# Optimization experiments

Measured on AMD Instinct MI355X. Metric: run time of the kernel, lower is better.

Reference implementation:

```python
import jax, jax.numpy as jnp
import numpy as np

B, T, X_DIM, H_DIM, C_NUM = 64, 1380, 96, 192, 345
SCALE = 1.0 / (X_DIM ** 0.5 * H_DIM ** 0.5)


def setup_inputs() -> dict:
    key = jax.random.key(0)
    k1, k2, k3, k4 = jax.random.split(key, 4)
    X = jax.random.normal(k1, (B, T, X_DIM), dtype=jnp.float32)
    H = jax.random.normal(k2, (B, T, H_DIM), dtype=jnp.float32)
    W1 = jax.random.normal(k3, (X_DIM, H_DIM), dtype=jnp.float32)
    W2 = jax.random.normal(k4, (C_NUM, T), dtype=jnp.float32)
    return {"X": X, "H": H, "W1": W1, "W2": W2}


def reference(X, H, W1, W2):
    # X: [B,T,x_dim] -> project to h_dim
    Xp = jnp.einsum('btx,xh->bth', X, W1)                 # [B,T,h]
    # batch_dot(X, H, axes=[2,2]) / sqrt(x_dim*h_dim)
    A = jnp.einsum('bth,buh->btu', Xp, H) * SCALE         # [B,T,T]
    # K.dot(W2, A) -> [c,B,T], then permute (1,0,2) -> [B,c,T]
    A = jnp.einsum('ct,btu->bcu', W2, A)                  # [B,c,T]
    A = jax.nn.softmax(A, axis=-1)
    # batch_dot(A, H, axes=[2,1])
    C = jnp.einsum('bcu,buh->bch', A, H)                  # [B,c,h]
    return C
```

## Files before the change

### kernel.cpp

```cpp
#include <hip/hip_runtime.h>
#include <math.h>

namespace {
constexpr int B_  = 64;
constexpr int T_  = 1380;
constexpr int XD_ = 96;
constexpr int HD_ = 192;
constexpr int CN_ = 345;
constexpr int CP_ = 384;
constexpr int TP_ = 1392;
constexpr int TP2_ = 1408;
constexpr int TH_ = 690;
constexpr float SCALE_ = 0.00736569563735987f;
}

typedef __attribute__((ext_vector_type(8))) short bf16x8;
typedef __attribute__((ext_vector_type(4))) float f32x4;
typedef unsigned short u16;
typedef unsigned int   u32;

__device__ __forceinline__ u16 f2bf(float f) {
    union { float f; u32 u; } c; c.f = f;
    u32 r = (c.u + 0x7fffu + ((c.u >> 16) & 1u)) >> 16;
    return (u16)r;
}
__device__ __forceinline__ float bf2f(u16 s) {
    union { u32 u; float f; } c; c.u = ((u32)s) << 16;
    return c.f;
}

__device__ __forceinline__ float red16_max(float v) {
    int ti;
    ti = __builtin_amdgcn_update_dpp(0, __builtin_bit_cast(int, v), 0x128, 0xf, 0xf, true);
    v = fmaxf(v, __builtin_bit_cast(float, ti));
    ti = __builtin_amdgcn_update_dpp(0, __builtin_bit_cast(int, v), 0x124, 0xf, 0xf, true);
    v = fmaxf(v, __builtin_bit_cast(float, ti));
    ti = __builtin_amdgcn_update_dpp(0, __builtin_bit_cast(int, v), 0x122, 0xf, 0xf, true);
    v = fmaxf(v, __builtin_bit_cast(float, ti));
    ti = __builtin_amdgcn_update_dpp(0, __builtin_bit_cast(int, v), 0x121, 0xf, 0xf, true);
    v = fmaxf(v, __builtin_bit_cast(float, ti));
    return v;
}
__device__ __forceinline__ float red16_sum(float v) {
    int ti;
    ti = __builtin_amdgcn_update_dpp(0, __builtin_bit_cast(int, v), 0x128, 0xf, 0xf, true);
    v += __builtin_bit_cast(float, ti);
    ti = __builtin_amdgcn_update_dpp(0, __builtin_bit_cast(int, v), 0x124, 0xf, 0xf, true);
    v += __builtin_bit_cast(float, ti);
    ti = __builtin_amdgcn_update_dpp(0, __builtin_bit_cast(int, v), 0x122, 0xf, 0xf, true);
    v += __builtin_bit_cast(float, ti);
    ti = __builtin_amdgcn_update_dpp(0, __builtin_bit_cast(int, v), 0x121, 0xf, 0xf, true);
    v += __builtin_bit_cast(float, ti);
    return v;
}

__global__ __launch_bounds__(256) void k0_h(const float* __restrict__ Hg,
                                            u16* __restrict__ Hh,
                                            u16* __restrict__ Hl,
                                            u16* __restrict__ Hth) {
    __shared__ u16 til[64][68];
    const int tid = threadIdx.x;
    const int u0 = blockIdx.x * 64, h0 = blockIdx.y * 64, b = blockIdx.z;
#pragma unroll
    for (int i = 0; i < 8; i++) {
        int lin = i * 256 + tid;
        int r = lin >> 5;
        int cp = lin & 31;
        int u = u0 + r, h = h0 + cp * 2;
        float2 v = make_float2(0.f, 0.f);
        if (u < T_) v = *(const float2*)(Hg + ((size_t)b * T_ + u) * HD_ + h);
        u16 hx = f2bf(v.x), hy = f2bf(v.y);
        u16 lx = f2bf(v.x - bf2f(hx)), ly = f2bf(v.y - bf2f(hy));
        if (u < T_) {
            *(u32*)(Hh + ((size_t)b * T_ + u) * HD_ + h) = (u32)hx | ((u32)hy << 16);
            *(u32*)(Hl + ((size_t)b * T_ + u) * HD_ + h) = (u32)lx | ((u32)ly << 16);
        }
        til[cp * 2][r]     = hx;
        til[cp * 2 + 1][r] = hy;
    }
    __syncthreads();
#pragma unroll
    for (int i = 0; i < 4; i++) {
        int lin = i * 256 + tid;
        int hh = lin >> 4, cc = lin & 15;
        int u = u0 + cc * 4;
        if (u + 4 <= T_) {
            ushort4 v;
            v.x = til[hh][cc * 4 + 0];
            v.y = til[hh][cc * 4 + 1];
            v.z = til[hh][cc * 4 + 2];
            v.w = til[hh][cc * 4 + 3];
            *(ushort4*)(Hth + ((size_t)b * HD_ + h0 + hh) * TP_ + u) = v;
        }
    }
}

__global__ __launch_bounds__(256) void k0_x(const float* __restrict__ Xg,
                                            u16* __restrict__ Xth,
                                            u16* __restrict__ Xtl) {
    __shared__ __align__(16) u16 tih[96][72];
    __shared__ __align__(16) u16 til[96][72];
    const int tid = threadIdx.x;
    const int t0 = blockIdx.x * 64, b = blockIdx.y;
#pragma unroll
    for (int i = 0; i < 24; i++) {
        int lin = i * 256 + tid;
        int r = lin / 96, x = lin % 96;
        float v = (t0 + r < T_) ? Xg[((size_t)b * T_ + t0 + r) * XD_ + x] : 0.f;
        u16 hi = f2bf(v);
        tih[x][r] = hi;
        til[x][r] = f2bf(v - bf2f(hi));
    }
    __syncthreads();
#pragma unroll
    for (int i = 0; i < 6; i++) {
        int id = i * 256 + tid;
        int buf = (id >= 768);
        int cid = buf ? id - 768 : id;
        int x = cid >> 3, col = cid & 7;
        uint4 v = *(const uint4*)&(buf ? til : tih)[x][col * 8];
        u16* dst = (buf ? Xtl : Xth) + ((size_t)b * XD_ + x) * TP2_ + t0 + col * 8;
        *(uint4*)dst = v;
    }
}

__global__ __launch_bounds__(256) void k0_w2(const float* __restrict__ W2g,
                                             u16* __restrict__ W2h,
                                             u16* __restrict__ W2l) {
    const int n = CP_ * (TP2_ / 2);
    for (int i = blockIdx.x * 256 + threadIdx.x; i < n; i += gridDim.x * 256) {
        int c = i / (TP2_ / 2), tc = i % (TP2_ / 2);
        int t = tc * 2;
        float v0 = 0.f, v1 = 0.f;
        if (c < CN_) {
            if (t < T_)     v0 = W2g[(size_t)c * T_ + t];
            if (t + 1 < T_) v1 = W2g[(size_t)c * T_ + t + 1];
        }
        u16 h0 = f2bf(v0), h1 = f2bf(v1);
        u16 l0 = f2bf(v0 - bf2f(h0)), l1 = f2bf(v1 - bf2f(h1));
        ((u32*)W2h)[i] = (u32)h0 | ((u32)h1 << 16);
        ((u32*)W2l)[i] = (u32)l0 | ((u32)l1 << 16);
    }
}

__global__ __launch_bounds__(256) void k0_w1(const float* __restrict__ W1g,
                                             u16* __restrict__ W1th,
                                             u16* __restrict__ W1tl) {
    int i = blockIdx.x * 256 + threadIdx.x;
    if (i < HD_ * XD_) {
        int h = i / XD_, x = i % XD_;
        float v = W1g[(size_t)x * HD_ + h];
        u16 hi = f2bf(v);
        W1th[i] = hi;
        W1tl[i] = f2bf(v - bf2f(hi));
    }
}

__global__ __launch_bounds__(256, 1) void k12_mfma(const u16* __restrict__ W2h,
                                                   const u16* __restrict__ W2l,
                                                   const u16* __restrict__ Xth,
                                                   const u16* __restrict__ Xtl,
                                                   const u16* __restrict__ W1th,
                                                   const u16* __restrict__ W1tl,
                                                   u32* __restrict__ Ysi) {
    __shared__ __align__(16) u16 smem[49152];
    float* sZ = (float*)smem;

    const int tid  = threadIdx.x;
    const int lane = tid & 63;
    const int w    = tid >> 6;
    const int tx   = lane & 15;
    const int quad = lane >> 4;
    const int wr   = w >> 1;
    const int wc2  = w & 1;
    const int L    = blockIdx.x;
    const int xcd  = L & 7;
    const int slot = L >> 3;
    const int b    = xcd * 8 + (slot >> 2);
    const int c0   = (slot & 3) * 96;

    const u16* gsrc;
    size_t rowstart;
    if (w == 0)      { gsrc = W2h; rowstart = (size_t)c0; }
    else if (w == 1) { gsrc = W2l; rowstart = (size_t)c0; }
    else if (w == 2) { gsrc = Xth; rowstart = (size_t)b * XD_; }
    else             { gsrc = Xtl; rowstart = (size_t)b * XD_; }
    const int jg = (lane & 7) ^ ((lane >> 3) & 7);

#define STAGE(bufsel, kk)                                                         \
    {                                                                             \
        u16* lb = smem + (bufsel) * 24576 + w * 6144;                             \
        _Pragma("unroll")                                                         \
        for (int i_ = 0; i_ < 12; i_++) {                                         \
            int row_ = i_ * 8 + (lane >> 3);                                      \
            const u16* gp_ = gsrc + (rowstart + row_) * TP2_ + (kk) + jg * 8;     \
            __builtin_amdgcn_global_load_lds(                                     \
                (const __attribute__((address_space(1))) u32*)(const void*)gp_,   \
                (__attribute__((address_space(3))) u32*)(void*)(lb + i_ * 512),   \
                16, 0, 0);                                                        \
        }                                                                         \
    }

    f32x4 accZ[3][3];
#pragma unroll
    for (int i = 0; i < 3; i++)
#pragma unroll
        for (int j = 0; j < 3; j++) accZ[i][j] = (f32x4){0.f, 0.f, 0.f, 0.f};

    STAGE(0, 0);
    for (int s = 0; s < 22; s++) {
        __builtin_amdgcn_sched_barrier(0);
        if (s < 21) {
            STAGE((s + 1) & 1, (s + 1) * 64);
            asm volatile("s_waitcnt vmcnt(12)" ::: "memory");
        } else {
            asm volatile("s_waitcnt vmcnt(0)" ::: "memory");
        }
        __builtin_amdgcn_s_barrier();
        __builtin_amdgcn_sched_barrier(0);
        const u16* bufp = smem + (s & 1) * 24576;
#pragma unroll
        for (int ks2 = 0; ks2 < 2; ks2++) {
            const int G = ks2 * 4 + quad;
            bf16x8 ah[3], al[3], bh3[3], bl3[3];
#pragma unroll
            for (int am = 0; am < 3; am++) {
                int row = wr * 48 + am * 16 + tx;
                int off = row * 64 + (G ^ (row & 7)) * 8;
                ah[am] = *(const bf16x8*)(bufp + off);
                al[am] = *(const bf16x8*)(bufp + 6144 + off);
            }
#pragma unroll
            for (int bn = 0; bn < 3; bn++) {
                int row = wc2 * 48 + bn * 16 + tx;
                int off = row * 64 + (G ^ (row & 7)) * 8;
                bh3[bn] = *(const bf16x8*)(bufp + 12288 + off);
                bl3[bn] = *(const bf16x8*)(bufp + 18432 + off);
            }
#pragma unroll
            for (int am = 0; am < 3; am++)
#pragma unroll
                for (int bn = 0; bn < 3; bn++) {
                    accZ[am][bn] = __builtin_amdgcn_mfma_f32_16x16x32_bf16(ah[am], bh3[bn], accZ[am][bn], 0, 0, 0);
                    accZ[am][bn] = __builtin_amdgcn_mfma_f32_16x16x32_bf16(ah[am], bl3[bn], accZ[am][bn], 0, 0, 0);
                    accZ[am][bn] = __builtin_amdgcn_mfma_f32_16x16x32_bf16(al[am], bh3[bn], accZ[am][bn], 0, 0, 0);
                }
        }
        asm volatile("s_waitcnt lgkmcnt(0)" ::: "memory");
        __builtin_amdgcn_sched_barrier(0);
        __builtin_amdgcn_s_barrier();
    }
#undef STAGE

    __builtin_amdgcn_sched_barrier(0);
#pragma unroll
    for (int am = 0; am < 3; am++)
#pragma unroll
        for (int bn = 0; bn < 3; bn++)
#pragma unroll
            for (int r = 0; r < 4; r++)
                sZ[(wr * 48 + am * 16 + quad * 4 + r) * 100 + wc2 * 48 + bn * 16 + tx] = accZ[am][bn][r];
    __syncthreads();

    bf16x8 A2h[3][3], A2l[3][3];
#pragma unroll
    for (int am = 0; am < 3; am++)
#pragma unroll
        for (int ks = 0; ks < 3; ks++) {
            const float* zrow = sZ + (wr * 48 + am * 16 + tx) * 100 + ks * 32 + quad * 8;
            bf16x8 vh, vl;
#pragma unroll
            for (int j = 0; j < 8; j++) {
                float v = zrow[j];
                u16 hi = f2bf(v);
                vh[j] = (short)hi;
                vl[j] = (short)f2bf(v - bf2f(hi));
            }
            A2h[am][ks] = vh; A2l[am][ks] = vl;
        }

    f32x4 accY[3][6];
#pragma unroll
    for (int i = 0; i < 3; i++)
#pragma unroll
        for (int j = 0; j < 6; j++) accY[i][j] = (f32x4){0.f, 0.f, 0.f, 0.f};
#pragma unroll
    for (int hn = 0; hn < 6; hn++) {
        const int hrow = wc2 * 96 + hn * 16 + tx;
#pragma unroll
        for (int ks = 0; ks < 3; ks++) {
            bf16x8 bh = *(const bf16x8*)(W1th + (size_t)hrow * XD_ + ks * 32 + quad * 8);
            bf16x8 bl = *(const bf16x8*)(W1tl + (size_t)hrow * XD_ + ks * 32 + quad * 8);
#pragma unroll
            for (int am = 0; am < 3; am++) {
                accY[am][hn] = __builtin_amdgcn_mfma_f32_16x16x32_bf16(A2h[am][ks], bh, accY[am][hn], 0, 0, 0);
                accY[am][hn] = __builtin_amdgcn_mfma_f32_16x16x32_bf16(A2h[am][ks], bl, accY[am][hn], 0, 0, 0);
                accY[am][hn] = __builtin_amdgcn_mfma_f32_16x16x32_bf16(A2l[am][ks], bh, accY[am][hn], 0, 0, 0);
            }
        }
    }

#pragma unroll
    for (int am = 0; am < 3; am++)
#pragma unroll
        for (int r = 0; r < 4; r++) {
            int c = c0 + wr * 48 + am * 16 + quad * 4 + r;
            if (c < CN_) {
                size_t base = ((size_t)b * CN_ + c) * HD_;
#pragma unroll
                for (int hn = 0; hn < 6; hn++) {
                    float y = SCALE_ * accY[am][hn][r];
                    u16 hi = f2bf(y);
                    u16 lo = f2bf(y - bf2f(hi));
                    Ysi[base + wc2 * 96 + hn * 16 + tx] = (u32)hi | ((u32)lo << 16);
                }
            }
        }
}

__global__ __launch_bounds__(768, 3) void k3_mfma(const u32* __restrict__ Ysi,
                                                  const u16* __restrict__ Hh,
                                                  const u16* __restrict__ Hl,
                                                  const u16* __restrict__ Hth,
                                                  float* __restrict__ Op,
                                                  float* __restrict__ Ml,
                                                  float* __restrict__ Ll) {
    __shared__ __align__(16) u16 smem[44544];

    const int tid  = threadIdx.x;
    const int lane = tid & 63;
    const int w    = tid >> 6;
    const int tx   = lane & 15;
    const int quad = lane >> 4;
    const int L    = blockIdx.x;
    const int xcd  = L & 7;
    const int slot = L >> 3;
    const int gp   = xcd * 16 + (slot >> 1);
    const int ct   = slot & 1;
    const int b    = gp >> 1;
    const int sp   = gp & 1;
    const int c0   = ct * 192;
    const int us   = sp * TH_, ue = us + TH_;

    bf16x8 Ah[6], Al[6];
    const int ar = c0 + w * 16 + tx;
    if (ar < CN_) {
        const u32* yi = Ysi + ((size_t)b * CN_ + ar) * HD_;
#pragma unroll
        for (int ks = 0; ks < 6; ks++) {
            u32 vv[8];
            *(uint4*)&vv[0] = *(const uint4*)(yi + ks * 32 + quad * 8);
            *(uint4*)&vv[4] = *(const uint4*)(yi + ks * 32 + quad * 8 + 4);
            bf16x8 hh, ll;
#pragma unroll
            for (int j = 0; j < 8; j++) {
                hh[j] = (short)(vv[j] & 0xffffu);
                ll[j] = (short)(vv[j] >> 16);
            }
            Ah[ks] = hh; Al[ks] = ll;
        }
    } else {
#pragma unroll
        for (int ks = 0; ks < 6; ks++) { Ah[ks] = (bf16x8)0; Al[ks] = (bf16x8)0; }
    }

    float m_s[4], l_s[4];
    f32x4 accO[12];
#pragma unroll
    for (int r = 0; r < 4; r++) { m_s[r] = -1e30f; l_s[r] = 0.f; }
#pragma unroll
    for (int j = 0; j < 12; j++) accO[j] = (f32x4){0.f, 0.f, 0.f, 0.f};

    const char* srcp[3];
    u32 off0[3];
    const u32 incw = (u32)__builtin_amdgcn_readfirstlane((w < 8) ? (32 * HD_ * 2) : 64);
#pragma unroll
    for (int j = 0; j < 3; j++) {
        int k = w * 3 + j;
        u32 o;
        if (k < 24) {
            int arr = (k < 12) ? 0 : 1;
            int ii  = k - arr * 12;
            int cid = ii * 64 + lane;
            int u   = cid / 24, c1 = cid % 24;
            int c   = (c1 & ~7) | ((c1 & 7) ^ ((u >> 1) & 7));
            const u16* basep = (arr == 0 ? Hh : Hl) + (size_t)b * T_ * HD_;
            srcp[j] = (const char*)basep + ((size_t)(us + u) * HD_ + c * 8) * 2;
            o = (u32)(arr * 24576 + ii * 1024);
        } else {
            int ii  = k - 24;
            int cid = ii * 64 + lane;
            int h   = cid >> 2, c2 = cid & 3;
            int c   = c2 ^ ((h >> 2) & 3);
            const u16* basep = Hth + (size_t)b * HD_ * TP_;
            srcp[j] = (const char*)basep + ((size_t)h * TP_ + us + c * 8) * 2;
            o = (u32)(49152 + ii * 1024);
        }
        off0[j] = (u32)__builtin_amdgcn_readfirstlane((int)o);
    }

#define STAGE3(bufsel)                                                            \
    {                                                                             \
        _Pragma("unroll")                                                         \
        for (int j_ = 0; j_ < 3; j_++) {                                          \
            __builtin_amdgcn_global_load_lds(                                     \
                (const __attribute__((address_space(1))) u32*)(const void*)srcp[j_], \
                (__attribute__((address_space(3))) u32*)(void*)((char*)smem + off0[j_] + (bufsel) * 12288), \
                16, 0, 0);                                                        \
            srcp[j_] += incw;                                                     \
        }                                                                         \
    }

    u16* sPb = smem + 36864;

    STAGE3(0);
    for (int t = 0; t < 22; t++) {
        const int u0  = us + t * 32;
        const int buf = t & 1;
        __builtin_amdgcn_sched_barrier(0);
        if (t < 21) {
            STAGE3(buf ^ 1);
            asm volatile("s_waitcnt vmcnt(3)" ::: "memory");
        } else {
            asm volatile("s_waitcnt vmcnt(0)" ::: "memory");
        }
        __builtin_amdgcn_s_barrier();
        __builtin_amdgcn_sched_barrier(0);

        const u16* Hhb = smem + buf * 6144;
        const u16* Hlb = smem + 12288 + buf * 6144;
        const u16* Htb = smem + 24576 + buf * 6144;

        f32x4 s0a = {0.f, 0.f, 0.f, 0.f}, s1a = {0.f, 0.f, 0.f, 0.f};
        f32x4 s0b = {0.f, 0.f, 0.f, 0.f}, s1b = {0.f, 0.f, 0.f, 0.f};
        const int xr = (tx >> 1) & 7;
        __builtin_amdgcn_s_setprio(1);
#pragma unroll
        for (int ks = 0; ks < 6; ks++) {
            const int cc = ks * 4 + quad;
            const int cs = (cc & ~7) | ((cc & 7) ^ xr);
            const int ro0 = tx * 192 + cs * 8;
            const int ro1 = (16 + tx) * 192 + cs * 8;
            bf16x8 bh0 = *(const bf16x8*)(Hhb + ro0);
            bf16x8 bl0 = *(const bf16x8*)(Hlb + ro0);
            bf16x8 bh1 = *(const bf16x8*)(Hhb + ro1);
            bf16x8 bl1 = *(const bf16x8*)(Hlb + ro1);
            s0a = __builtin_amdgcn_mfma_f32_16x16x32_bf16(Ah[ks], bh0, s0a, 0, 0, 0);
            s1a = __builtin_amdgcn_mfma_f32_16x16x32_bf16(Ah[ks], bl0, s1a, 0, 0, 0);
            s1a = __builtin_amdgcn_mfma_f32_16x16x32_bf16(Al[ks], bh0, s1a, 0, 0, 0);
            s0b = __builtin_amdgcn_mfma_f32_16x16x32_bf16(Ah[ks], bh1, s0b, 0, 0, 0);
            s1b = __builtin_amdgcn_mfma_f32_16x16x32_bf16(Ah[ks], bl1, s1b, 0, 0, 0);
            s1b = __builtin_amdgcn_mfma_f32_16x16x32_bf16(Al[ks], bh1, s1b, 0, 0, 0);
        }
        __builtin_amdgcn_s_setprio(0);
        float sv0[4], sv1[4];
        const bool okA = (u0 + tx) < ue, okB = (u0 + 16 + tx) < ue;
#pragma unroll
        for (int r = 0; r < 4; r++) {
            sv0[r] = okA ? (s0a[r] + s1a[r]) : -1e30f;
            sv1[r] = okB ? (s0b[r] + s1b[r]) : -1e30f;
        }

        float alpha[4];
#pragma unroll
        for (int r = 0; r < 4; r++) {
            float mx = red16_max(fmaxf(sv0[r], sv1[r]));
            float mn = fmaxf(m_s[r], mx);
            alpha[r] = __expf(m_s[r] - mn);
            float p0 = __expf(sv0[r] - mn);
            float p1 = __expf(sv1[r] - mn);
            sPb[(w * 16 + quad * 4 + r) * 40 + tx]      = f2bf(p0);
            sPb[(w * 16 + quad * 4 + r) * 40 + 16 + tx] = f2bf(p1);
            float s = red16_sum(p0 + p1);
            l_s[r] = l_s[r] * alpha[r] + s;
            m_s[r] = mn;
        }
        f32x4 alv = {alpha[0], alpha[1], alpha[2], alpha[3]};
#pragma unroll
        for (int j = 0; j < 12; j++) accO[j] *= alv;

        bf16x8 pa = *(const bf16x8*)(sPb + (w * 16 + tx) * 40 + quad * 8);
        const int ctq = quad ^ ((tx >> 2) & 3);
        __builtin_amdgcn_s_setprio(1);
#pragma unroll
        for (int j = 0; j < 12; j++) {
            bf16x8 hb = *(const bf16x8*)(Htb + (j * 16 + tx) * 32 + ctq * 8);
            accO[j] = __builtin_amdgcn_mfma_f32_16x16x32_bf16(pa, hb, accO[j], 0, 0, 0);
        }
        __builtin_amdgcn_s_setprio(0);

        asm volatile("s_waitcnt lgkmcnt(0)" ::: "memory");
        __builtin_amdgcn_sched_barrier(0);
        __builtin_amdgcn_s_barrier();
    }
#undef STAGE3

#pragma unroll
    for (int r = 0; r < 4; r++) {
        int c = c0 + w * 16 + quad * 4 + r;
        if (c < CN_) {
            float* orow = Op + (((size_t)sp * B_ + b) * CN_ + c) * HD_;
#pragma unroll
            for (int j = 0; j < 12; j++) orow[j * 16 + tx] = accO[j][r];
            if (tx == 0) {
                size_t mi = ((size_t)sp * B_ + b) * CN_ + c;
                Ml[mi] = m_s[r];
                Ll[mi] = l_s[r];
            }
        }
    }
}

__global__ __launch_bounds__(192) void k_merge(const float* __restrict__ Op,
                                               const float* __restrict__ Ml,
                                               const float* __restrict__ Ll,
                                               float* __restrict__ out) {
    const int c = blockIdx.x, b = blockIdx.y, h = threadIdx.x;
    const size_t i0 = (size_t)b * CN_ + c;
    const size_t i1 = (size_t)B_ * CN_ + i0;
    float m0 = Ml[i0], m1 = Ml[i1];
    float l0 = Ll[i0], l1 = Ll[i1];
    float M  = fmaxf(m0, m1);
    float e0 = __expf(m0 - M), e1 = __expf(m1 - M);
    float L  = l0 * e0 + l1 * e1;
    float o0 = Op[i0 * HD_ + h], o1 = Op[i1 * HD_ + h];
    out[i0 * HD_ + h] = (o0 * e0 + o1 * e1) / L;
}

extern "C" void kernel_launch(void* const* d_in, const int* in_sizes, int n_in,
                              void* d_out, int out_size, void* d_ws, size_t ws_size,
                              hipStream_t stream) {
    const float* X  = (const float*)d_in[0];
    const float* H  = (const float*)d_in[1];
    const float* W1 = (const float*)d_in[2];
    const float* W2 = (const float*)d_in[3];
    float* out = (float*)d_out;

    char* ws = (char*)d_ws;
    u32*   Ysi  = (u32*)(ws);
    u16*   Hh   = (u16*)(ws + 16957440);
    u16*   Hl   = (u16*)(ws + 50872320);
    u16*   Hth  = (u16*)(ws + 84787200);
    u16*   Xth  = (u16*)(ws + 118996992);
    u16*   Xtl  = (u16*)(ws + 136298496);
    float* Op   = (float*)(ws + 118996992);
    u16*   W2h  = (u16*)(ws + 153600000);
    u16*   W2l  = (u16*)(ws + 154681344);
    u16*   W1th = (u16*)(ws + 155762688);
    u16*   W1tl = (u16*)(ws + 155799552);
    float* Ml   = (float*)(ws + 155836416);
    float* Ll   = (float*)(ws + 156013056);

    k0_h    <<<dim3(22, 3, B_), 256, 0, stream>>>(H, Hh, Hl, Hth);
    k0_x    <<<dim3(22, B_),    256, 0, stream>>>(X, Xth, Xtl);
    k0_w2   <<<dim3(1056),      256, 0, stream>>>(W2, W2h, W2l);
    k0_w1   <<<dim3(72),        256, 0, stream>>>(W1, W1th, W1tl);
    k12_mfma<<<dim3(256),       256, 0, stream>>>(W2h, W2l, Xth, Xtl, W1th, W1tl, Ysi);
    k3_mfma <<<dim3(256),       768, 0, stream>>>(Ysi, Hh, Hl, Hth, Op, Ml, Ll);
    k_merge <<<dim3(CN_, B_),   192, 0, stream>>>(Op, Ml, Ll, out);
}
```

Before: 284.6 us.

## Warp-specialize attention kernel into score/softmax and PV-accumulate wave groups

```diff
diff --git a/kernel.cpp b/kernel.cpp
--- a/kernel.cpp
+++ b/kernel.cpp
@@ -325,7 +325,7 @@
                                                   float* __restrict__ Op,
                                                   float* __restrict__ Ml,
                                                   float* __restrict__ Ll) {
-    __shared__ __align__(16) u16 smem[44544];
+    __shared__ __align__(16) u16 smem[59136];
 
     const int tid  = threadIdx.x;
     const int lane = tid & 63;
@@ -341,35 +341,6 @@
     const int sp   = gp & 1;
     const int c0   = ct * 192;
     const int us   = sp * TH_, ue = us + TH_;
-
-    bf16x8 Ah[6], Al[6];
-    const int ar = c0 + w * 16 + tx;
-    if (ar < CN_) {
-        const u32* yi = Ysi + ((size_t)b * CN_ + ar) * HD_;
-#pragma unroll
-        for (int ks = 0; ks < 6; ks++) {
-            u32 vv[8];
-            *(uint4*)&vv[0] = *(const uint4*)(yi + ks * 32 + quad * 8);
-            *(uint4*)&vv[4] = *(const uint4*)(yi + ks * 32 + quad * 8 + 4);
-            bf16x8 hh, ll;
-#pragma unroll
-            for (int j = 0; j < 8; j++) {
-                hh[j] = (short)(vv[j] & 0xffffu);
-                ll[j] = (short)(vv[j] >> 16);
-            }
-            Ah[ks] = hh; Al[ks] = ll;
-        }
-    } else {
-#pragma unroll
-        for (int ks = 0; ks < 6; ks++) { Ah[ks] = (bf16x8)0; Al[ks] = (bf16x8)0; }
-    }
-
-    float m_s[4], l_s[4];
-    f32x4 accO[12];
-#pragma unroll
-    for (int r = 0; r < 4; r++) { m_s[r] = -1e30f; l_s[r] = 0.f; }
-#pragma unroll
-    for (int j = 0; j < 12; j++) accO[j] = (f32x4){0.f, 0.f, 0.f, 0.f};
 
     const char* srcp[3];
     u32 off0[3];
@@ -399,116 +370,201 @@
         off0[j] = (u32)__builtin_amdgcn_readfirstlane((int)o);
     }
 
-#define STAGE3(bufsel)                                                            \
+#define STAGE3(b2, b3)                                                            \
     {                                                                             \
+        const u32 bofs_ = ((w < 8) ? (u32)(b2) : (u32)(b3)) * 12288u;             \
         _Pragma("unroll")                                                         \
         for (int j_ = 0; j_ < 3; j_++) {                                          \
             __builtin_amdgcn_global_load_lds(                                     \
                 (const __attribute__((address_space(1))) u32*)(const void*)srcp[j_], \
-                (__attribute__((address_space(3))) u32*)(void*)((char*)smem + off0[j_] + (bufsel) * 12288), \
+                (__attribute__((address_space(3))) u32*)(void*)((char*)smem + off0[j_] + bofs_), \
                 16, 0, 0);                                                        \
             srcp[j_] += incw;                                                     \
         }                                                                         \
     }
 
-    u16* sPb = smem + 36864;
-
-    STAGE3(0);
-    for (int t = 0; t < 22; t++) {
-        const int u0  = us + t * 32;
-        const int buf = t & 1;
-        __builtin_amdgcn_sched_barrier(0);
-        if (t < 21) {
-            STAGE3(buf ^ 1);
-            asm volatile("s_waitcnt vmcnt(3)" ::: "memory");
-        } else {
-            asm volatile("s_waitcnt vmcnt(0)" ::: "memory");
-        }
-        __builtin_amdgcn_s_barrier();
-        __builtin_amdgcn_sched_barrier(0);
-
-        const u16* Hhb = smem + buf * 6144;
-        const u16* Hlb = smem + 12288 + buf * 6144;
-        const u16* Htb = smem + 24576 + buf * 6144;
-
-        f32x4 s0a = {0.f, 0.f, 0.f, 0.f}, s1a = {0.f, 0.f, 0.f, 0.f};
-        f32x4 s0b = {0.f, 0.f, 0.f, 0.f}, s1b = {0.f, 0.f, 0.f, 0.f};
-        const int xr = (tx >> 1) & 7;
-        __builtin_amdgcn_s_setprio(1);
-#pragma unroll
-        for (int ks = 0; ks < 6; ks++) {
-            const int cc = ks * 4 + quad;
-            const int cs = (cc & ~7) | ((cc & 7) ^ xr);
-            const int ro0 = tx * 192 + cs * 8;
-            const int ro1 = (16 + tx) * 192 + cs * 8;
-            bf16x8 bh0 = *(const bf16x8*)(Hhb + ro0);
-            bf16x8 bl0 = *(const bf16x8*)(Hlb + ro0);
-            bf16x8 bh1 = *(const bf16x8*)(Hhb + ro1);
-            bf16x8 bl1 = *(const bf16x8*)(Hlb + ro1);
-            s0a = __builtin_amdgcn_mfma_f32_16x16x32_bf16(Ah[ks], bh0, s0a, 0, 0, 0);
-            s1a = __builtin_amdgcn_mfma_f32_16x16x32_bf16(Ah[ks], bl0, s1a, 0, 0, 0);
-            s1a = __builtin_amdgcn_mfma_f32_16x16x32_bf16(Al[ks], bh0, s1a, 0, 0, 0);
-            s0b = __builtin_amdgcn_mfma_f32_16x16x32_bf16(Ah[ks], bh1, s0b, 0, 0, 0);
-            s1b = __builtin_amdgcn_mfma_f32_16x16x32_bf16(Ah[ks], bl1, s1b, 0, 0, 0);
-            s1b = __builtin_amdgcn_mfma_f32_16x16x32_bf16(Al[ks], bh1, s1b, 0, 0, 0);
-        }
-        __builtin_amdgcn_s_setprio(0);
-        float sv0[4], sv1[4];
-        const bool okA = (u0 + tx) < ue, okB = (u0 + 16 + tx) < ue;
-#pragma unroll
-        for (int r = 0; r < 4; r++) {
-            sv0[r] = okA ? (s0a[r] + s1a[r]) : -1e30f;
-            sv1[r] = okB ? (s0b[r] + s1b[r]) : -1e30f;
-        }
-
-        float alpha[4];
-#pragma unroll
-        for (int r = 0; r < 4; r++) {
-            float mx = red16_max(fmaxf(sv0[r], sv1[r]));
-            float mn = fmaxf(m_s[r], mx);
-            alpha[r] = __expf(m_s[r] - mn);
-            float p0 = __expf(sv0[r] - mn);
-            float p1 = __expf(sv1[r] - mn);
-            sPb[(w * 16 + quad * 4 + r) * 40 + tx]      = f2bf(p0);
-            sPb[(w * 16 + quad * 4 + r) * 40 + 16 + tx] = f2bf(p1);
-            float s = red16_sum(p0 + p1);
-            l_s[r] = l_s[r] * alpha[r] + s;
-            m_s[r] = mn;
-        }
-        f32x4 alv = {alpha[0], alpha[1], alpha[2], alpha[3]};
-#pragma unroll
-        for (int j = 0; j < 12; j++) accO[j] *= alv;
-
-        bf16x8 pa = *(const bf16x8*)(sPb + (w * 16 + tx) * 40 + quad * 8);
-        const int ctq = quad ^ ((tx >> 2) & 3);
-        __builtin_amdgcn_s_setprio(1);
-#pragma unroll
-        for (int j = 0; j < 12; j++) {
-            bf16x8 hb = *(const bf16x8*)(Htb + (j * 16 + tx) * 32 + ctq * 8);
-            accO[j] = __builtin_amdgcn_mfma_f32_16x16x32_bf16(pa, hb, accO[j], 0, 0, 0);
-        }
-        __builtin_amdgcn_s_setprio(0);
-
-        asm volatile("s_waitcnt lgkmcnt(0)" ::: "memory");
-        __builtin_amdgcn_sched_barrier(0);
-        __builtin_amdgcn_s_barrier();
+#define PVSTEP(tt)                                                                \
+    {                                                                             \
+        const int pb_ = (tt) & 1, h3_ = (tt) % 3;                                 \
+        const float* aB_ = (const float*)((const char*)smem + 116736 + pb_ * 768);\
+        f32x4 al0 = *(const f32x4*)(aB_ + cw * 32 + quad * 4);                    \
+        f32x4 al1 = *(const f32x4*)(aB_ + cw * 32 + 16 + quad * 4);               \
+        _Pragma("unroll")                                                         \
+        for (int j_ = 0; j_ < 12; j_++) { accO[0][j_] *= al0; accO[1][j_] *= al1; } \
+        const u16* sPc_ = smem + 43008 + pb_ * 7680;                              \
+        bf16x8 pa0 = *(const bf16x8*)(sPc_ + (cw * 32 + tx) * 40 + quad * 8);     \
+        bf16x8 pa1 = *(const bf16x8*)(sPc_ + (cw * 32 + 16 + tx) * 40 + quad * 8);\
+        const u16* Htb_ = smem + 24576 + h3_ * 6144;                              \
+        const int ctq_ = quad ^ ((tx >> 2) & 3);                                  \
+        __builtin_amdgcn_s_setprio(1);                                            \
+        _Pragma("unroll")                                                         \
+        for (int j_ = 0; j_ < 12; j_++) {                                         \
+            bf16x8 hb_ = *(const bf16x8*)(Htb_ + (j_ * 16 + tx) * 32 + ctq_ * 8); \
+            accO[0][j_] = __builtin_amdgcn_mfma_f32_16x16x32_bf16(pa0, hb_, accO[0][j_], 0, 0, 0); \
+            accO[1][j_] = __builtin_amdgcn_mfma_f32_16x16x32_bf16(pa1, hb_, accO[1][j_], 0, 0, 0); \
+        }                                                                         \
+        __builtin_amdgcn_s_setprio(0);                                            \
+    }
+
+    if (w < 6) {
+        bf16x8 Ah2[2][6], Al2[2][6];
+#pragma unroll
+        for (int st = 0; st < 2; st++) {
+            const int ar = c0 + w * 32 + st * 16 + tx;
+            if (ar < CN_) {
+                const u32* yi = Ysi + ((size_t)b * CN_ + ar) * HD_;
+#pragma unroll
+                for (int ks = 0; ks < 6; ks++) {
+                    u32 vv[8];
+                    *(uint4*)&vv[0] = *(const uint4*)(yi + ks * 32 + quad * 8);
+                    *(uint4*)&vv[4] = *(const uint4*)(yi + ks * 32 + quad * 8 + 4);
+                    bf16x8 hh, ll;
+#pragma unroll
+                    for (int j = 0; j < 8; j++) {
+                        hh[j] = (short)(vv[j] & 0xffffu);
+                        ll[j] = (short)(vv[j] >> 16);
+                    }
+                    Ah2[st][ks] = hh; Al2[st][ks] = ll;
+                }
+            } else {
+#pragma unroll
+                for (int ks = 0; ks < 6; ks++) { Ah2[st][ks] = (bf16x8)0; Al2[st][ks] = (bf16x8)0; }
+            }
+        }
+        float m_s[2][4], l_s[2][4];
+#pragma unroll
+        for (int st = 0; st < 2; st++)
+#pragma unroll
+            for (int r = 0; r < 4; r++) { m_s[st][r] = -1e30f; l_s[st][r] = 0.f; }
+
+        STAGE3(0, 0);
+        for (int t = 0; t < 22; t++) {
+            const int u0 = us + t * 32;
+            __builtin_amdgcn_sched_barrier(0);
+            if (t < 21) {
+                STAGE3((t + 1) & 1, (t + 1) % 3);
+                asm volatile("s_waitcnt vmcnt(3)" ::: "memory");
+            } else {
+                asm volatile("s_waitcnt vmcnt(0)" ::: "memory");
+            }
+            __builtin_amdgcn_s_barrier();
+            __builtin_amdgcn_sched_barrier(0);
+
+            const u16* Hhb = smem + (t & 1) * 6144;
+            const u16* Hlb = smem + 12288 + (t & 1) * 6144;
+            const int xr = (tx >> 1) & 7;
+            f32x4 sv0[2], sv1[2];
+#pragma unroll
+            for (int half = 0; half < 2; half++) {
+                f32x4 s0[2], s1[2];
+#pragma unroll
+                for (int st = 0; st < 2; st++) { s0[st] = (f32x4){0.f,0.f,0.f,0.f}; s1[st] = (f32x4){0.f,0.f,0.f,0.f}; }
+                const int ub = half * 16 + tx;
+                __builtin_amdgcn_s_setprio(1);
+#pragma unroll
+                for (int ks = 0; ks < 6; ks++) {
+                    const int cc = ks * 4 + quad;
+                    const int cs = (cc & ~7) | ((cc & 7) ^ xr);
+                    const int ro = ub * 192 + cs * 8;
+                    bf16x8 bh = *(const bf16x8*)(Hhb + ro);
+                    bf16x8 bl = *(const bf16x8*)(Hlb + ro);
+#pragma unroll
+                    for (int st = 0; st < 2; st++) {
+                        s0[st] = __builtin_amdgcn_mfma_f32_16x16x32_bf16(Ah2[st][ks], bh, s0[st], 0, 0, 0);
+                        s1[st] = __builtin_amdgcn_mfma_f32_16x16x32_bf16(Ah2[st][ks], bl, s1[st], 0, 0, 0);
+                        s1[st] = __builtin_amdgcn_mfma_f32_16x16x32_bf16(Al2[st][ks], bh, s1[st], 0, 0, 0);
+                    }
+                }
+                __builtin_amdgcn_s_setprio(0);
+                const bool ok = (u0 + ub) < ue;
+#pragma unroll
+                for (int st = 0; st < 2; st++)
+#pragma unroll
+                    for (int r = 0; r < 4; r++) {
+                        float v = ok ? (s0[st][r] + s1[st][r]) : -1e30f;
+                        if (half == 0) sv0[st][r] = v; else sv1[st][r] = v;
+                    }
+            }
+
+            u16*   sPb = smem + 43008 + (t & 1) * 7680;
+            float* aB  = (float*)((char*)smem + 116736 + (t & 1) * 768);
+#pragma unroll
+            for (int st = 0; st < 2; st++)
+#pragma unroll
+                for (int r = 0; r < 4; r++) {
+                    float mx = red16_max(fmaxf(sv0[st][r], sv1[st][r]));
+                    float mn = fmaxf(m_s[st][r], mx);
+                    float alpha = __expf(m_s[st][r] - mn);
+                    float p0 = __expf(sv0[st][r] - mn);
+                    float p1 = __expf(sv1[st][r] - mn);
+                    const int row = w * 32 + st * 16 + quad * 4 + r;
+                    sPb[row * 40 + tx]      = f2bf(p0);
+                    sPb[row * 40 + 16 + tx] = f2bf(p1);
+                    aB[row] = alpha;
+                    float s = red16_sum(p0 + p1);
+                    l_s[st][r] = l_s[st][r] * alpha + s;
+                    m_s[st][r] = mn;
+                }
+
+            asm volatile("s_waitcnt lgkmcnt(0)" ::: "memory");
+            __builtin_amdgcn_sched_barrier(0);
+            __builtin_amdgcn_s_barrier();
+        }
+        if (tx == 0) {
+#pragma unroll
+            for (int st = 0; st < 2; st++)
+#pragma unroll
+                for (int r = 0; r < 4; r++) {
+                    int c = c0 + w * 32 + st * 16 + quad * 4 + r;
+                    if (c < CN_) {
+                        size_t mi = ((size_t)sp * B_ + b) * CN_ + c;
+                        Ml[mi] = m_s[st][r];
+                        Ll[mi] = l_s[st][r];
+                    }
+                }
+        }
+    } else {
+        const int cw = w - 6;
+        f32x4 accO[2][12];
+#pragma unroll
+        for (int st = 0; st < 2; st++)
+#pragma unroll
+            for (int j = 0; j < 12; j++) accO[st][j] = (f32x4){0.f, 0.f, 0.f, 0.f};
+
+        STAGE3(0, 0);
+        for (int t = 0; t < 22; t++) {
+            __builtin_amdgcn_sched_barrier(0);
+            if (t < 21) {
+                STAGE3((t + 1) & 1, (t + 1) % 3);
+                asm volatile("s_waitcnt vmcnt(3)" ::: "memory");
+            } else {
+                asm volatile("s_waitcnt vmcnt(0)" ::: "memory");
+            }
+            __builtin_amdgcn_s_barrier();
+            __builtin_amdgcn_sched_barrier(0);
+
+            if (t > 0) { PVSTEP(t - 1) }
+
+            asm volatile("s_waitcnt lgkmcnt(0)" ::: "memory");
+            __builtin_amdgcn_sched_barrier(0);
+            __builtin_amdgcn_s_barrier();
+        }
+        PVSTEP(21)
+
+#pragma unroll
+        for (int st = 0; st < 2; st++)
+#pragma unroll
+            for (int r = 0; r < 4; r++) {
+                int c = c0 + cw * 32 + st * 16 + quad * 4 + r;
+                if (c < CN_) {
+                    float* orow = Op + (((size_t)sp * B_ + b) * CN_ + c) * HD_;
+#pragma unroll
+                    for (int j = 0; j < 12; j++) orow[j * 16 + tx] = accO[st][j][r];
+                }
+            }
     }
 #undef STAGE3
-
-#pragma unroll
-    for (int r = 0; r < 4; r++) {
-        int c = c0 + w * 16 + quad * 4 + r;
-        if (c < CN_) {
-            float* orow = Op + (((size_t)sp * B_ + b) * CN_ + c) * HD_;
-#pragma unroll
-            for (int j = 0; j < 12; j++) orow[j * 16 + tx] = accO[j][r];
-            if (tx == 0) {
-                size_t mi = ((size_t)sp * B_ + b) * CN_ + c;
-                Ml[mi] = m_s[r];
-                Ll[mi] = l_s[r];
-            }
-        }
-    }
+#undef PVSTEP
 }
 
 __global__ __launch_bounds__(192) void k_merge(const float* __restrict__ Op,
```

Result: slower. 292.4 us (+2.7%).
